# Kernel tuning notes

Hardware: AMD Instinct MI355X
Metric: run time of the kernel (lower is better)

## Reference

```python
import jax, jax.numpy as jnp
import numpy as np

N_PLAYERS = 1_000_000
N_MAPS = 200_000
EMBED_DIM = 64
BATCH = 1_000_000


def setup_inputs() -> dict:
    key = jax.random.key(0)
    k1, k2, k3, k4 = jax.random.split(key, 4)
    player_indices = jax.random.randint(k1, (BATCH,), 0, N_PLAYERS, dtype=jnp.int64 if jax.config.jax_enable_x64 else jnp.int32)
    map_indices = jax.random.randint(k2, (BATCH,), 0, N_MAPS, dtype=jnp.int64 if jax.config.jax_enable_x64 else jnp.int32)
    # nn.init.normal_(std=0.1) for players; torch.randn * 0.1 for maps -> both N(0, 0.1)
    player_table = jax.random.normal(k3, (N_PLAYERS, EMBED_DIM), dtype=jnp.float32) * 0.1
    map_table = jax.random.normal(k4, (N_MAPS, EMBED_DIM), dtype=jnp.float32) * 0.1
    return {
        "player_indices": player_indices,
        "map_indices": map_indices,
        "player_table": player_table,
        "map_table": map_table,
    }


def reference(player_indices, map_indices, player_table, map_table):
    # Gather per-sample embeddings, elementwise multiply, sum over embed dim.
    player_emb = player_table[player_indices]  # [B, D]
    map_emb = map_table[map_indices]           # [B, D]
    predicted_rating = jnp.sum(player_emb * map_emb, axis=-1)  # [B]
    return predicted_rating
```

## Files before the change

kernel.cpp:

```cpp
#include <hip/hip_runtime.h>


__global__ __launch_bounds__(256) void osu_rating_dot_kernel(
    const int* __restrict__ pidx,
    const int* __restrict__ midx,
    const float* __restrict__ ptab,
    const float* __restrict__ mtab,
    float* __restrict__ out,
    int n)
{
    int tid = blockIdx.x * blockDim.x + threadIdx.x;
    int sample = tid >> 4;
    int lane4  = tid & 15;
    if (sample >= n) return;

    int pi = pidx[sample];
    int mi = midx[sample];

    const float4 pv = *reinterpret_cast<const float4*>(ptab + (size_t)pi * 64 + (size_t)lane4 * 4);
    const float4 mv = *reinterpret_cast<const float4*>(mtab + (size_t)mi * 64 + (size_t)lane4 * 4);

    float s = pv.x * mv.x + pv.y * mv.y + pv.z * mv.z + pv.w * mv.w;

    s += __shfl_xor(s, 1, 16);
    s += __shfl_xor(s, 2, 16);
    s += __shfl_xor(s, 4, 16);
    s += __shfl_xor(s, 8, 16);

    if (lane4 == 0) out[sample] = s;
}

extern "C" void kernel_launch(void* const* d_in, const int* in_sizes, int n_in,
                              void* d_out, int out_size, void* d_ws, size_t ws_size,
                              hipStream_t stream) {
    const int*   pidx = (const int*)d_in[0];
    const int*   midx = (const int*)d_in[1];
    const float* ptab = (const float*)d_in[2];
    const float* mtab = (const float*)d_in[3];
    float*       out  = (float*)d_out;

    int n = in_sizes[0];
    int total_threads = n * 16;
    int block = 256;
    int grid = (total_threads + block - 1) / block;

    osu_rating_dot_kernel<<<grid, block, 0, stream>>>(pidx, midx, ptab, mtab, out, n);
}
```

Measured before the change: 75.63 us.

## Bucket samples by map index before gathering to improve map-table cache locality

Measured after the change: 260.8 us. 245% more time.

```diff
diff --git a/kernel.cpp b/kernel.cpp
--- a/kernel.cpp
+++ b/kernel.cpp
@@ -1,24 +1,77 @@
 #include <hip/hip_runtime.h>
 
 
-__global__ __launch_bounds__(256) void osu_rating_dot_kernel(
-    const int* __restrict__ pidx,
-    const int* __restrict__ midx,
-    const float* __restrict__ ptab,
-    const float* __restrict__ mtab,
-    float* __restrict__ out,
-    int n)
-{
-    int tid = blockIdx.x * blockDim.x + threadIdx.x;
+#define NB 4096
+
+typedef float f4 __attribute__((ext_vector_type(4)));
+
+__global__ void k_zero(int* __restrict__ hist) {
+    int t = blockIdx.x * blockDim.x + threadIdx.x;
+    if (t < NB) hist[t] = 0;
+}
+
+__global__ __launch_bounds__(256) void k_hist(const int* __restrict__ midx,
+                                              int* __restrict__ hist, int n, int shift) {
+    int i = blockIdx.x * blockDim.x + threadIdx.x;
+    int stride = gridDim.x * blockDim.x;
+    for (; i < n; i += stride)
+        atomicAdd(&hist[midx[i] >> shift], 1);
+}
+
+__global__ __launch_bounds__(1024) void k_scan(const int* __restrict__ hist,
+                                               int* __restrict__ cursor) {
+    __shared__ int lds[1024];
+    int t = threadIdx.x;
+    int4 h = *reinterpret_cast<const int4*>(hist + t * 4);
+    int s0 = h.x, s1 = s0 + h.y, s2 = s1 + h.z, s3 = s2 + h.w;
+    lds[t] = s3;
+    __syncthreads();
+    for (int off = 1; off < 1024; off <<= 1) {
+        int x = (t >= off) ? lds[t - off] : 0;
+        __syncthreads();
+        lds[t] += x;
+        __syncthreads();
+    }
+    int prefix = (t > 0) ? lds[t - 1] : 0;
+    int4 e;
+    e.x = prefix; e.y = prefix + s0; e.z = prefix + s1; e.w = prefix + s2;
+    *reinterpret_cast<int4*>(cursor + t * 4) = e;
+}
+
+__global__ __launch_bounds__(256) void k_scatter(
+    const int* __restrict__ pidx, const int* __restrict__ midx,
+    int* __restrict__ cursor,
+    int* __restrict__ rp, int* __restrict__ rm, int* __restrict__ rs,
+    int n, int shift) {
+    int i = blockIdx.x * blockDim.x + threadIdx.x;
+    int stride = gridDim.x * blockDim.x;
+    for (; i < n; i += stride) {
+        int mi = midx[i];
+        int pos = atomicAdd(&cursor[mi >> shift], 1);
+        rp[pos] = pidx[i];
+        rm[pos] = mi;
+        rs[pos] = i;
+    }
+}
+
+__global__ __launch_bounds__(256) void k_process(
+    const int* __restrict__ rp, const int* __restrict__ rm, const int* __restrict__ rs,
+    const float* __restrict__ ptab, const float* __restrict__ mtab,
+    float* __restrict__ out, int n, int q, int r) {
+    int o = blockIdx.x;
+    int xcd = o & 7, idx = o >> 3;
+    int wg = (xcd < r) ? xcd * (q + 1) + idx : r * (q + 1) + (xcd - r) * q + idx;
+
+    int tid = wg * 256 + (int)threadIdx.x;
     int sample = tid >> 4;
-    int lane4  = tid & 15;
+    int lane4 = tid & 15;
     if (sample >= n) return;
 
-    int pi = pidx[sample];
-    int mi = midx[sample];
+    int pi = rp[sample];
+    int mi = rm[sample];
 
-    const float4 pv = *reinterpret_cast<const float4*>(ptab + (size_t)pi * 64 + (size_t)lane4 * 4);
-    const float4 mv = *reinterpret_cast<const float4*>(mtab + (size_t)mi * 64 + (size_t)lane4 * 4);
+    f4 pv = *reinterpret_cast<const f4*>(ptab + (size_t)pi * 64 + (size_t)lane4 * 4);
+    f4 mv = *reinterpret_cast<const f4*>(mtab + (size_t)mi * 64 + (size_t)lane4 * 4);
 
     float s = pv.x * mv.x + pv.y * mv.y + pv.z * mv.z + pv.w * mv.w;
 
@@ -27,6 +80,26 @@
     s += __shfl_xor(s, 4, 16);
     s += __shfl_xor(s, 8, 16);
 
+    if (lane4 == 0) out[rs[sample]] = s;
+}
+
+__global__ __launch_bounds__(256) void k_direct(
+    const int* __restrict__ pidx, const int* __restrict__ midx,
+    const float* __restrict__ ptab, const float* __restrict__ mtab,
+    float* __restrict__ out, int n) {
+    int tid = blockIdx.x * blockDim.x + threadIdx.x;
+    int sample = tid >> 4;
+    int lane4 = tid & 15;
+    if (sample >= n) return;
+    int pi = pidx[sample];
+    int mi = midx[sample];
+    f4 pv = *reinterpret_cast<const f4*>(ptab + (size_t)pi * 64 + (size_t)lane4 * 4);
+    f4 mv = *reinterpret_cast<const f4*>(mtab + (size_t)mi * 64 + (size_t)lane4 * 4);
+    float s = pv.x * mv.x + pv.y * mv.y + pv.z * mv.z + pv.w * mv.w;
+    s += __shfl_xor(s, 1, 16);
+    s += __shfl_xor(s, 2, 16);
+    s += __shfl_xor(s, 4, 16);
+    s += __shfl_xor(s, 8, 16);
     if (lane4 == 0) out[sample] = s;
 }
 
@@ -40,9 +113,31 @@
     float*       out  = (float*)d_out;
 
     int n = in_sizes[0];
-    int total_threads = n * 16;
-    int block = 256;
-    int grid = (total_threads + block - 1) / block;
+    int nmaps = in_sizes[3] / 64;
 
-    osu_rating_dot_kernel<<<grid, block, 0, stream>>>(pidx, midx, ptab, mtab, out, n);
+    size_t need = (size_t)(2 * NB + 3 * (size_t)n) * sizeof(int);
+    if (ws_size < need) {
+        int total = n * 16;
+        k_direct<<<(total + 255) / 256, 256, 0, stream>>>(pidx, midx, ptab, mtab, out, n);
+        return;
+    }
+
+    int shift = 0;
+    while (((nmaps - 1) >> shift) >= NB) shift++;
+
+    int* hist   = (int*)d_ws;
+    int* cursor = hist + NB;
+    int* rp     = cursor + NB;
+    int* rm     = rp + n;
+    int* rs     = rm + n;
+
+    k_zero<<<(NB + 255) / 256, 256, 0, stream>>>(hist);
+    k_hist<<<2048, 256, 0, stream>>>(midx, hist, n, shift);
+    k_scan<<<1, 1024, 0, stream>>>(hist, cursor);
+    k_scatter<<<2048, 256, 0, stream>>>(pidx, midx, cursor, rp, rm, rs, n, shift);
+
+    int total = n * 16;
+    int nwg = (total + 255) / 256;
+    int q = nwg / 8, r = nwg % 8;
+    k_process<<<nwg, 256, 0, stream>>>(rp, rm, rs, ptab, mtab, out, n, q, r);
 }
```
